# Performance work log

Measured on AMD Instinct MI355X. Metric: run time of the kernel, lower is better.

The kernel has to match this reference:

```python
import jax, jax.numpy as jnp
import numpy as np

N_MICS = 8
MIC_RADIUS = 0.05
SAMPLE_RATE = 16000.0
SPEED_SOUND = 343.0
EPS = 1e-20
SPHERE_LEVELS = 4


def sphere_np(levels=SPHERE_LEVELS):
    # Faithful numpy port of the torch icosphere subdivision in sphere().
    h = 5.0 ** 0.5 / 5.0
    r = 2.0 / 5.0 * 5.0 ** 0.5
    pi = 3.141592654
    pts = np.zeros((12, 3), dtype=np.float32)
    pts[0] = [0.0, 0.0, 1.0]
    pts[11] = [0.0, 0.0, -1.0]
    k = np.arange(5, dtype=np.float32)
    pts[1:6, 0] = r * np.sin(2.0 * pi * k / 5.0)
    pts[1:6, 1] = r * np.cos(2.0 * pi * k / 5.0)
    pts[1:6, 2] = h
    pts[6:11, 0] = -r * np.sin(2.0 * pi * k / 5.0)
    pts[6:11, 1] = -r * np.cos(2.0 * pi * k / 5.0)
    pts[6:11, 2] = -h
    trs = np.array([[0, 2, 1], [0, 3, 2], [0, 4, 3], [0, 5, 4], [0, 1, 5],
                    [9, 1, 2], [10, 2, 3], [6, 3, 4], [7, 4, 5], [8, 5, 1],
                    [4, 7, 6], [5, 8, 7], [1, 9, 8], [2, 10, 9], [3, 6, 10],
                    [11, 6, 7], [11, 7, 8], [11, 8, 9], [11, 9, 10], [11, 10, 6]], dtype=np.int64)
    for _ in range(levels):
        T = trs.shape[0]
        sub = np.zeros((4 * T, 6), dtype=np.int64)
        sub[0 * T:1 * T] = trs[:, [0, 0, 0, 1, 2, 0]]
        sub[1 * T:2 * T] = trs[:, [0, 1, 1, 1, 1, 2]]
        sub[2 * T:3 * T] = trs[:, [2, 0, 1, 2, 2, 2]]
        sub[3 * T:4 * T] = trs[:, [0, 1, 1, 2, 2, 0]]
        flat = np.concatenate((sub[:, [0, 1]], sub[:, [2, 3]], sub[:, [4, 5]]), axis=0)
        srt = np.sort(flat, axis=1)
        m = srt.max()
        scal = srt[:, 0] * (m + 1) + srt[:, 1]
        uniq, inv = np.unique(scal, return_inverse=True)
        uv0 = uniq // (m + 1)
        uv1 = uniq - uv0 * (m + 1)
        trs = inv.reshape(3, -1).T
        pts = pts[uv0] + pts[uv1]
        pts /= np.sqrt((pts ** 2).sum(axis=1, keepdims=True))
    return pts.astype(np.float32)


def setup_inputs() -> dict:
    key = jax.random.key(0)
    # DOA grid and TDOAs from array geometry (precomputed in SrpPhat.__init__)
    doas_np = sphere_np()                                    # [2562, 3]
    ang = 2.0 * np.pi * np.arange(N_MICS) / N_MICS
    mics_np = np.stack([MIC_RADIUS * np.cos(ang), MIC_RADIUS * np.sin(ang),
                        np.zeros(N_MICS)], axis=1).astype(np.float32)  # [8, 3]
    taus_np = (SAMPLE_RATE / SPEED_SOUND) * (doas_np @ mics_np.T)      # [2562, 8]
    B, T, F, P = 4, 250, 513, N_MICS * (N_MICS + 1) // 2
    XXs = jax.random.normal(key, (B, T, F, 2, P), dtype=jnp.float32)
    return {"XXs": XXs, "taus": jnp.asarray(taus_np), "doas": jnp.asarray(doas_np)}


def reference(XXs, taus, doas):
    B, T, F, _, P = XXs.shape
    n_mics = taus.shape[1]
    D = taus.shape[0]
    frame_size = (F - 1) * 2
    # Steering phases: a = exp(-j * omega * tau)   [D, F, M]
    omegas = 2.0 * jnp.pi * jnp.arange(F, dtype=jnp.float32) / frame_size
    phase = omegas[None, :, None] * taus[:, None, :]
    A_re = jnp.cos(phase)
    A_im = -jnp.sin(phase)
    # Cross steering terms for every mic pair (triu incl. diagonal): W = a_i * conj(a_j)^H form
    i0, i1 = np.triu_indices(n_mics)                         # 36 pairs for 8 mics
    Ws_re = A_re[:, :, i0] * A_re[:, :, i1] + A_im[:, :, i0] * A_im[:, :, i1]  # [D, F, P]
    Ws_im = A_re[:, :, i0] * A_im[:, :, i1] - A_im[:, :, i0] * A_re[:, :, i1]
    # PHAT normalization of the cross-spectra
    XX_re = XXs[:, :, :, 0, :]
    XX_im = XXs[:, :, :, 1, :]
    mag = jnp.sqrt(XX_re ** 2 + XX_im ** 2) + EPS
    Xr = (XX_re / mag).reshape(B, T, F * P)
    Xi = (XX_im / mag).reshape(B, T, F * P)
    Wr = Ws_re.reshape(D, F * P)
    Wi = Ws_im.reshape(D, F * P)
    # SRP map: Re{ sum_fp XX_norm * conj(W) } reduced over freqs and pairs
    Ys = jnp.matmul(Xr, Wr.T) + jnp.matmul(Xi, Wi.T)         # [B, T, D]
    idx = jnp.argmax(Ys, axis=2)                             # [B, T]
    return doas[idx]                                         # [B, T, 3]
```

## Files before the change

kernel.cpp:

```cpp
#include <hip/hip_runtime.h>
#include <math.h>


#define F_BINS  513
#define M_TOTAL 1000
#define D_TOTAL 2562
#define D_PAD   2688
#define NPAIR   28
#define NC      32
#define K2      (NPAIR * NC)
#define S_SCALE 4.67f
#define KSPB    2
#define KPS     448

#define OFF_COEF 0
#define OFF_TT   16512
#define OFF_G    (OFF_TT + (size_t)K2 * D_PAD)
#define OFF_YS   (OFF_G + (size_t)M_TOTAL * K2)

__device__ __constant__ int c_ptab[NPAIR] = {1,2,3,4,5,6,7, 9,10,11,12,13,14,
                                             16,17,18,19,20, 22,23,24,25,
                                             27,28,29, 31,32, 34};
__device__ __constant__ int c_i0[NPAIR] = {0,0,0,0,0,0,0, 1,1,1,1,1,1,
                                           2,2,2,2,2, 3,3,3,3, 4,4,4, 5,5, 6};
__device__ __constant__ int c_i1[NPAIR] = {1,2,3,4,5,6,7, 2,3,4,5,6,7,
                                           3,4,5,6,7, 4,5,6,7, 5,6,7, 6,7, 7};

__global__ void k_coef(float* __restrict__ coefEO) {
    __shared__ double sHC[NC][NC + 1];
    __shared__ double sHS[NC][NC + 1];
    const int f = blockIdx.x;
    const int t = threadIdx.x;
    const double z = (double)f * (M_PI / 512.0) * (double)S_SCALE;
    double th = M_PI * (t + 0.5) / NC;
    double ct = cos(th);
    double hs, hc;
    sincos(z * ct, &hs, &hc);
    double cp = 1.0, cc = ct, c2 = 2.0 * ct;
    sHC[0][t] = hc;      sHS[0][t] = hs;
    sHC[1][t] = hc * cc; sHS[1][t] = hs * cc;
    for (int n = 2; n < NC; ++n) {
        double cn = c2 * cc - cp;
        cp = cc; cc = cn;
        sHC[n][t] = hc * cn;
        sHS[n][t] = hs * cn;
    }
    __syncthreads();
    const int n = (t < 16) ? 2 * t : 2 * (t - 16) + 1;
    double sum = 0.0;
    if (t < 16) { for (int j = 0; j < NC; ++j) sum += sHC[n][j]; }
    else        { for (int j = 0; j < NC; ++j) sum += sHS[n][j]; }
    double scale = (n == 0) ? (1.0 / NC) : (2.0 / NC);
    coefEO[f * 32 + t] = (float)(sum * scale);
}

__global__ void k_ttab(const float* __restrict__ taus, float* __restrict__ Tt) {
    const int d = blockIdx.x * 256 + threadIdx.x;
    const int p = blockIdx.y;
    if (d >= D_PAD) return;
    const bool live = d < D_TOTAL;
    const int dd = live ? d : 0;
    const float u = (taus[dd * 8 + c_i0[p]] - taus[dd * 8 + c_i1[p]]) * (1.0f / S_SCALE);
    float* base = Tt + (size_t)p * 32 * D_PAD + d;
    base[0] = live ? 1.f : 0.f;
    base[(size_t)16 * D_PAD] = live ? u : 0.f;
    float tp = 1.f, tc = u;
    const float u2 = 2.f * u;
    for (int n = 2; n < NC; ++n) {
        float tn = u2 * tc - tp;
        tp = tc; tc = tn;
        int c = (n & 1) ? 16 + (n >> 1) : (n >> 1);
        base[(size_t)c * D_PAD] = live ? tn : 0.f;
    }
}

__global__ __launch_bounds__(256) void k_stageA(
    const float* __restrict__ XXs, const float* __restrict__ coefEO,
    float* __restrict__ G)
{
    __shared__ float sRaw[32][72];
    __shared__ float sXn[32][64];
    __shared__ float sC[32][32];
    const int bt = blockIdx.x;
    const int t  = threadIdx.x;
    const int p   = t & 31;
    const int sel = t >> 5;
    const bool im = sel >= 4;
    const int row = p + (im ? 32 : 0);
    const int c0  = (sel & 3) * 4 + (im ? 16 : 0);
    const float* xb = XXs + (size_t)bt * F_BINS * 72;
    float acc[4] = {};

    for (int f0 = 0; f0 < F_BINS; f0 += 32) {
        const int cnt = min(32, F_BINS - f0);
        __syncthreads();
        for (int e = t; e < cnt * 8; e += 256)
            *(float4*)&sC[0][e * 4] = *(const float4*)&coefEO[f0 * 32 + e * 4];
        for (int e = t; e < cnt * 18; e += 256) {
            int fl = e / 18, q = e - fl * 18;
            *(float4*)&sRaw[fl][q * 4] = *(const float4*)&xb[(size_t)(f0 + fl) * 72 + q * 4];
        }
        __syncthreads();
        for (int e = t; e < cnt * 28; e += 256) {
            int fl = e / 28, pp = e - fl * 28;
            int po = c_ptab[pp];
            float xr = sRaw[fl][po];
            float xi = sRaw[fl][36 + po];
            float inv = 1.f / (sqrtf(xr * xr + xi * xi) + 1e-20f);
            sXn[fl][pp]      = xr * inv;
            sXn[fl][32 + pp] = xi * inv;
        }
        __syncthreads();
        for (int fl = 0; fl < cnt; ++fl) {
            float a = sXn[fl][row];
            float4 c4 = *(const float4*)&sC[fl][c0];
            acc[0] = fmaf(a, c4.x, acc[0]);
            acc[1] = fmaf(a, c4.y, acc[1]);
            acc[2] = fmaf(a, c4.z, acc[2]);
            acc[3] = fmaf(a, c4.w, acc[3]);
        }
    }
    if (p < NPAIR) {
        float4 v = {acc[0], acc[1], acc[2], acc[3]};
        *(float4*)&G[(size_t)bt * K2 + p * 32 + c0] = v;
    }
}

#define BKB 32
__global__ __launch_bounds__(256) void k_gemmB(
    const float* __restrict__ G, const float* __restrict__ Tt,
    float* __restrict__ Ysp)
{
    __shared__ float sAT[64][33];
    __shared__ float sB[BKB][68];
    const int t = threadIdx.x;
    const int row0  = blockIdx.x * 64;
    const int col0  = blockIdx.y * 64;
    const int koff  = blockIdx.z * KPS;
    const int tx = t & 15;
    const int ty = t >> 4;
    float acc[4][4] = {};

    for (int k0 = 0; k0 < KPS; k0 += BKB) {
        __syncthreads();
        for (int e = t; e < 64 * BKB; e += 256) {
            int r = e >> 5, kk = e & 31;
            int rg = row0 + r;
            sAT[r][kk] = (rg < M_TOTAL) ? G[(size_t)rg * K2 + koff + k0 + kk] : 0.f;
        }
        for (int e = t; e < 512; e += 256) {
            int kk = e >> 4, cq = e & 15;
            *(float4*)&sB[kk][cq * 4] =
                *(const float4*)&Tt[(size_t)(koff + k0 + kk) * D_PAD + col0 + cq * 4];
        }
        __syncthreads();
        #pragma unroll 8
        for (int kk = 0; kk < BKB; ++kk) {
            float a0 = sAT[ty * 4 + 0][kk];
            float a1 = sAT[ty * 4 + 1][kk];
            float a2 = sAT[ty * 4 + 2][kk];
            float a3 = sAT[ty * 4 + 3][kk];
            float4 b = *(const float4*)&sB[kk][tx * 4];
            float av[4] = {a0, a1, a2, a3};
            float bv[4] = {b.x, b.y, b.z, b.w};
            #pragma unroll
            for (int i = 0; i < 4; ++i)
                #pragma unroll
                for (int j = 0; j < 4; ++j)
                    acc[i][j] = fmaf(av[i], bv[j], acc[i][j]);
        }
    }
    float* yp = Ysp + (size_t)blockIdx.z * M_TOTAL * D_PAD;
    #pragma unroll
    for (int i = 0; i < 4; ++i) {
        int rg = row0 + ty * 4 + i;
        if (rg >= M_TOTAL) continue;
        float4 v = {acc[i][0], acc[i][1], acc[i][2], acc[i][3]};
        *(float4*)(yp + (size_t)rg * D_PAD + col0 + tx * 4) = v;
    }
}

__global__ __launch_bounds__(256) void k_argmax(
    const float* __restrict__ Ysp, const float* __restrict__ doas,
    float* __restrict__ out)
{
    __shared__ float sv[256];
    __shared__ int   si[256];
    const int row = blockIdx.x;
    const int tid = threadIdx.x;
    const float* y0 = Ysp + (size_t)row * D_PAD;
    const float* y1 = y0 + (size_t)M_TOTAL * D_PAD;
    float best = -INFINITY;
    int bi = D_TOTAL;
    for (int d = tid; d < D_TOTAL; d += 256) {
        float v = y0[d] + y1[d];
        if (v > best) { best = v; bi = d; }
    }
    sv[tid] = best; si[tid] = bi;
    __syncthreads();
    for (int s = 128; s > 0; s >>= 1) {
        if (tid < s) {
            float v2 = sv[tid + s]; int i2 = si[tid + s];
            if (v2 > sv[tid] || (v2 == sv[tid] && i2 < si[tid])) { sv[tid] = v2; si[tid] = i2; }
        }
        __syncthreads();
    }
    if (tid == 0) {
        int idx = si[0];
        out[row * 3 + 0] = doas[idx * 3 + 0];
        out[row * 3 + 1] = doas[idx * 3 + 1];
        out[row * 3 + 2] = doas[idx * 3 + 2];
    }
}

extern "C" void kernel_launch(void* const* d_in, const int* in_sizes, int n_in,
                              void* d_out, int out_size, void* d_ws, size_t ws_size,
                              hipStream_t stream) {
    const float* XXs  = (const float*)d_in[0];
    const float* taus = (const float*)d_in[1];
    const float* doas = (const float*)d_in[2];
    float* ws     = (float*)d_ws;
    float* coefEO = ws + OFF_COEF;
    float* Tt     = ws + OFF_TT;
    float* G      = ws + OFF_G;
    float* Ysp    = ws + OFF_YS;

    k_coef  <<<F_BINS, 32, 0, stream>>>(coefEO);
    k_ttab  <<<dim3((D_PAD + 255) / 256, NPAIR), 256, 0, stream>>>(taus, Tt);
    k_stageA<<<M_TOTAL, 256, 0, stream>>>(XXs, coefEO, G);
    k_gemmB <<<dim3(16, D_PAD / 64, KSPB), 256, 0, stream>>>(G, Tt, Ysp);
    k_argmax<<<M_TOTAL, 256, 0, stream>>>(Ysp, doas, (float*)d_out);
}
```

Before: 355.0 us.

## Batch frames and split frequencies in stage A; widen GEMM tile columns

Stage A now handles four frames per block, reusing each coefficient tile across them. It also splits the frequency range six ways across the grid to add parallelism, and a new reduction kernel sums the partial G buffers. The GEMM tile grows to 64x128 with 4x8 accumulators per thread to raise arithmetic intensity. The costs are an extra kernel launch, extra partial-buffer traffic, and more registers in the GEMM. Stage A also drops the coalesced staging of raw inputs in favour of strided global loads.

Result: slower. 387.7 us (+9.2%).

```diff
diff --git a/kernel.cpp b/kernel.cpp
--- a/kernel.cpp
+++ b/kernel.cpp
@@ -10,13 +10,16 @@
 #define NC      32
 #define K2      (NPAIR * NC)
 #define S_SCALE 4.67f
+#define NBT     4
+#define FSPLIT  6
 #define KSPB    2
 #define KPS     448
 
 #define OFF_COEF 0
 #define OFF_TT   16512
 #define OFF_G    (OFF_TT + (size_t)K2 * D_PAD)
-#define OFF_YS   (OFF_G + (size_t)M_TOTAL * K2)
+#define OFF_GP   (OFF_G + (size_t)M_TOTAL * K2)
+#define OFF_YS   OFF_GP
 
 __device__ __constant__ int c_ptab[NPAIR] = {1,2,3,4,5,6,7, 9,10,11,12,13,14,
                                              16,17,18,19,20, 22,23,24,25,
@@ -76,53 +79,71 @@
 
 __global__ __launch_bounds__(256) void k_stageA(
     const float* __restrict__ XXs, const float* __restrict__ coefEO,
-    float* __restrict__ G)
+    float* __restrict__ Gp)
 {
-    __shared__ float sRaw[32][72];
-    __shared__ float sXn[32][64];
-    __shared__ float sC[32][32];
-    const int bt = blockIdx.x;
-    const int t  = threadIdx.x;
+    __shared__ float sXn[16][NBT][64];
+    __shared__ float sC[16][32];
+    const int t     = threadIdx.x;
+    const int bt0   = blockIdx.x * NBT;
+    const int split = blockIdx.y;
+    const int fbeg  = (F_BINS * split) / FSPLIT;
+    const int fend  = (F_BINS * (split + 1)) / FSPLIT;
     const int p   = t & 31;
     const int sel = t >> 5;
     const bool im = sel >= 4;
     const int row = p + (im ? 32 : 0);
     const int c0  = (sel & 3) * 4 + (im ? 16 : 0);
-    const float* xb = XXs + (size_t)bt * F_BINS * 72;
-    float acc[4] = {};
-
-    for (int f0 = 0; f0 < F_BINS; f0 += 32) {
-        const int cnt = min(32, F_BINS - f0);
+    float acc[NBT][4] = {};
+
+    for (int fc = fbeg; fc < fend; fc += 16) {
+        const int cnt = min(16, fend - fc);
         __syncthreads();
         for (int e = t; e < cnt * 8; e += 256)
-            *(float4*)&sC[0][e * 4] = *(const float4*)&coefEO[f0 * 32 + e * 4];
-        for (int e = t; e < cnt * 18; e += 256) {
-            int fl = e / 18, q = e - fl * 18;
-            *(float4*)&sRaw[fl][q * 4] = *(const float4*)&xb[(size_t)(f0 + fl) * 72 + q * 4];
-        }
-        __syncthreads();
-        for (int e = t; e < cnt * 28; e += 256) {
-            int fl = e / 28, pp = e - fl * 28;
+            *(float4*)&sC[0][e * 4] = *(const float4*)&coefEO[fc * 32 + e * 4];
+        for (int e = t; e < NBT * cnt * 28; e += 256) {
+            int pp   = e % 28;
+            int rest = e / 28;
+            int fl   = rest % cnt;
+            int bt   = rest / cnt;
+            const float* bp = XXs + ((size_t)(bt0 + bt) * F_BINS + (fc + fl)) * 72;
             int po = c_ptab[pp];
-            float xr = sRaw[fl][po];
-            float xi = sRaw[fl][36 + po];
+            float xr = bp[po];
+            float xi = bp[36 + po];
             float inv = 1.f / (sqrtf(xr * xr + xi * xi) + 1e-20f);
-            sXn[fl][pp]      = xr * inv;
-            sXn[fl][32 + pp] = xi * inv;
+            sXn[fl][bt][pp]      = xr * inv;
+            sXn[fl][bt][32 + pp] = xi * inv;
         }
         __syncthreads();
         for (int fl = 0; fl < cnt; ++fl) {
-            float a = sXn[fl][row];
             float4 c4 = *(const float4*)&sC[fl][c0];
-            acc[0] = fmaf(a, c4.x, acc[0]);
-            acc[1] = fmaf(a, c4.y, acc[1]);
-            acc[2] = fmaf(a, c4.z, acc[2]);
-            acc[3] = fmaf(a, c4.w, acc[3]);
+            #pragma unroll
+            for (int bt = 0; bt < NBT; ++bt) {
+                float a = sXn[fl][bt][row];
+                acc[bt][0] = fmaf(a, c4.x, acc[bt][0]);
+                acc[bt][1] = fmaf(a, c4.y, acc[bt][1]);
+                acc[bt][2] = fmaf(a, c4.z, acc[bt][2]);
+                acc[bt][3] = fmaf(a, c4.w, acc[bt][3]);
+            }
         }
     }
     if (p < NPAIR) {
-        float4 v = {acc[0], acc[1], acc[2], acc[3]};
-        *(float4*)&G[(size_t)bt * K2 + p * 32 + c0] = v;
+        float* gsp = Gp + (size_t)split * M_TOTAL * K2;
+        #pragma unroll
+        for (int bt = 0; bt < NBT; ++bt) {
+            float4 v = {acc[bt][0], acc[bt][1], acc[bt][2], acc[bt][3]};
+            *(float4*)&gsp[(size_t)(bt0 + bt) * K2 + p * 32 + c0] = v;
+        }
+    }
+}
+
+__global__ void k_reduceG(const float* __restrict__ Gp, float* __restrict__ G) {
+    const int i = blockIdx.x * 256 + threadIdx.x;
+    const size_t MK = (size_t)M_TOTAL * K2;
+    if (i < (int)MK) {
+        float s = 0.f;
+        #pragma unroll
+        for (int k = 0; k < FSPLIT; ++k) s += Gp[i + k * MK];
+        G[i] = s;
     }
 }
 
@@ -132,14 +153,14 @@
     float* __restrict__ Ysp)
 {
     __shared__ float sAT[64][33];
-    __shared__ float sB[BKB][68];
+    __shared__ float sB[BKB][132];
     const int t = threadIdx.x;
-    const int row0  = blockIdx.x * 64;
-    const int col0  = blockIdx.y * 64;
-    const int koff  = blockIdx.z * KPS;
+    const int row0 = blockIdx.x * 64;
+    const int col0 = blockIdx.y * 128;
+    const int koff = blockIdx.z * KPS;
     const int tx = t & 15;
     const int ty = t >> 4;
-    float acc[4][4] = {};
+    float acc[4][8] = {};
 
     for (int k0 = 0; k0 < KPS; k0 += BKB) {
         __syncthreads();
@@ -148,25 +169,24 @@
             int rg = row0 + r;
             sAT[r][kk] = (rg < M_TOTAL) ? G[(size_t)rg * K2 + koff + k0 + kk] : 0.f;
         }
-        for (int e = t; e < 512; e += 256) {
-            int kk = e >> 4, cq = e & 15;
+        for (int e = t; e < 1024; e += 256) {
+            int kk = e >> 5, cq = e & 31;
             *(float4*)&sB[kk][cq * 4] =
                 *(const float4*)&Tt[(size_t)(koff + k0 + kk) * D_PAD + col0 + cq * 4];
         }
         __syncthreads();
         #pragma unroll 8
         for (int kk = 0; kk < BKB; ++kk) {
-            float a0 = sAT[ty * 4 + 0][kk];
-            float a1 = sAT[ty * 4 + 1][kk];
-            float a2 = sAT[ty * 4 + 2][kk];
-            float a3 = sAT[ty * 4 + 3][kk];
-            float4 b = *(const float4*)&sB[kk][tx * 4];
-            float av[4] = {a0, a1, a2, a3};
-            float bv[4] = {b.x, b.y, b.z, b.w};
+            float av[4];
+            #pragma unroll
+            for (int i = 0; i < 4; ++i) av[i] = sAT[ty * 4 + i][kk];
+            float4 b0 = *(const float4*)&sB[kk][tx * 8];
+            float4 b1 = *(const float4*)&sB[kk][tx * 8 + 4];
+            float bv[8] = {b0.x, b0.y, b0.z, b0.w, b1.x, b1.y, b1.z, b1.w};
             #pragma unroll
             for (int i = 0; i < 4; ++i)
                 #pragma unroll
-                for (int j = 0; j < 4; ++j)
+                for (int j = 0; j < 8; ++j)
                     acc[i][j] = fmaf(av[i], bv[j], acc[i][j]);
         }
     }
@@ -175,8 +195,11 @@
     for (int i = 0; i < 4; ++i) {
         int rg = row0 + ty * 4 + i;
         if (rg >= M_TOTAL) continue;
-        float4 v = {acc[i][0], acc[i][1], acc[i][2], acc[i][3]};
-        *(float4*)(yp + (size_t)rg * D_PAD + col0 + tx * 4) = v;
+        float* y = yp + (size_t)rg * D_PAD + col0 + tx * 8;
+        float4 v0 = {acc[i][0], acc[i][1], acc[i][2], acc[i][3]};
+        float4 v1 = {acc[i][4], acc[i][5], acc[i][6], acc[i][7]};
+        *(float4*)&y[0] = v0;
+        *(float4*)&y[4] = v1;
     }
 }
 
@@ -223,11 +246,13 @@
     float* coefEO = ws + OFF_COEF;
     float* Tt     = ws + OFF_TT;
     float* G      = ws + OFF_G;
+    float* Gp     = ws + OFF_GP;
     float* Ysp    = ws + OFF_YS;
 
-    k_coef  <<<F_BINS, 32, 0, stream>>>(coefEO);
-    k_ttab  <<<dim3((D_PAD + 255) / 256, NPAIR), 256, 0, stream>>>(taus, Tt);
-    k_stageA<<<M_TOTAL, 256, 0, stream>>>(XXs, coefEO, G);
-    k_gemmB <<<dim3(16, D_PAD / 64, KSPB), 256, 0, stream>>>(G, Tt, Ysp);
-    k_argmax<<<M_TOTAL, 256, 0, stream>>>(Ysp, doas, (float*)d_out);
-}
+    k_coef   <<<F_BINS, 32, 0, stream>>>(coefEO);
+    k_ttab   <<<dim3((D_PAD + 255) / 256, NPAIR), 256, 0, stream>>>(taus, Tt);
+    k_stageA <<<dim3(M_TOTAL / NBT, FSPLIT), 256, 0, stream>>>(XXs, coefEO, Gp);
+    k_reduceG<<<(M_TOTAL * K2 + 255) / 256, 256, 0, stream>>>(Gp, G);
+    k_gemmB  <<<dim3(16, D_PAD / 128, KSPB), 256, 0, stream>>>(G, Tt, Ysp);
+    k_argmax <<<M_TOTAL, 256, 0, stream>>>(Ysp, doas, (float*)d_out);
+}
```
